# Kernel optimization log

Hardware: AMD Instinct MI355X
Metric: run time of the kernel (lower is better)

Reference implementation:

```python
import jax, jax.numpy as jnp
import numpy as np

BS, NQ, NK = 4096, 21, 7   # batch, num_neg queries, 7 keys (weekdays)
E = 512                     # key_size == query_size
H = 512                     # hidden_size
NEG_INF = -1e9


def setup_inputs() -> dict:
    key = jax.random.key(0)
    ks = jax.random.split(key, 6)
    sq = 1.0 / np.sqrt(E)
    sh = 1.0 / np.sqrt(H)
    return {
        "queries": jax.random.normal(ks[0], (BS, NQ, E), jnp.float32),
        "keys": jax.random.normal(ks[1], (BS, NK, E), jnp.float32),
        "wq_w": jax.random.normal(ks[2], (H, E), jnp.float32) * sq,
        "wq_b": jnp.zeros((H,), jnp.float32),
        "wk_w": jax.random.normal(ks[3], (H, E), jnp.float32) * sq,
        "wk_b": jnp.zeros((H,), jnp.float32),
        "wv_w": jax.random.normal(ks[4], (1, H), jnp.float32) * sh,
        "wv_b": jnp.zeros((1,), jnp.float32),
        "cum_subs_masks": jax.random.randint(ks[5], (BS, 1, NK, 1), 0, 2).astype(jnp.int32),
        "num_neg": NQ,
    }


def reference(queries, keys, wq_w, wq_b, wk_w, wk_b, wv_w, wv_b, cum_subs_masks, num_neg):
    # dropout p=0.0 -> identity (as in eval / p=0)
    q = jnp.einsum('bqe,he->bqh', queries, wq_w) + wq_b          # (bs,21,H)
    k = jnp.einsum('bke,he->bkh', keys, wk_w) + wk_b             # (bs,7,H)
    # additive score: broadcast q over keys, k over queries
    t = jnp.tanh(q[:, :, None, :] + k[:, None, :, :])            # (bs,21,7,H)
    scores = jnp.einsum('bqkh,oh->bqko', t, wv_w) + wv_b         # (bs,21,7,1)
    scores = scores + cum_subs_masks.astype(scores.dtype) * NEG_INF
    attn_weights = jax.nn.softmax(scores, axis=-2)               # softmax over 7 keys
    # weighted sum of the RAW keys (the module multiplies by expanded `keys`)
    attn_out = jnp.einsum('bqk,bke->bqe', attn_weights[..., 0], keys)  # (bs,21,E)
    return (attn_out, attn_weights)
```

## Files before the change

kernel.cpp:

```cpp
#include <hip/hip_runtime.h>
#include <hip/hip_bf16.h>

#define BS_   4096
#define NQ_   21
#define NK_   7
#define E_    512
#define MQ_   (BS_*NQ_)
#define MK_   (BS_*NK_)
#define MT1_  (MQ_/128)
#define MT2_  (MK_/128)
#define SCALE_ 2.88539008177792681f

typedef __attribute__((ext_vector_type(8))) short bf16x8;
typedef __attribute__((ext_vector_type(4))) float f32x4;
typedef __attribute__((ext_vector_type(8))) unsigned short u16x8;

__device__ __forceinline__ unsigned int cvt_pk_bf16(float lo, float hi){
  unsigned int r;
  asm("v_cvt_pk_bf16_f32 %0, %1, %2" : "=v"(r) : "v"(lo), "v"(hi));
  return r;
}
__device__ __forceinline__ unsigned short f2bfu(float x){
  return __builtin_bit_cast(unsigned short, __float2bfloat16(x));
}
__device__ __forceinline__ float bf2f(unsigned short h){
  return __builtin_bit_cast(float, (unsigned int)h << 16);
}
__device__ __forceinline__ void gload_lds16(const void* g, void* l){
  __builtin_amdgcn_global_load_lds(
      (const __attribute__((address_space(1))) unsigned int*)g,
      (__attribute__((address_space(3))) unsigned int*)l, 16, 0, 0);
}

__global__ __launch_bounds__(256) void cast_weights(
    const float* __restrict__ wq, const float* __restrict__ wk,
    unsigned int* __restrict__ oq, unsigned int* __restrict__ ok)
{
  int i = blockIdx.x * 256 + threadIdx.x;
  float4 a = ((const float4*)wq)[i];
  float4 b = ((const float4*)wk)[i];
  uint2 ua = { cvt_pk_bf16(a.x, a.y), cvt_pk_bf16(a.z, a.w) };
  uint2 ub = { cvt_pk_bf16(b.x, b.y), cvt_pk_bf16(b.z, b.w) };
  ((uint2*)oq)[i] = ua;
  ((uint2*)ok)[i] = ub;
}

__global__ __launch_bounds__(256)
void gemm_proj(const float* __restrict__ Aq, const float* __restrict__ Ak,
               const unsigned short* __restrict__ Bq, const unsigned short* __restrict__ Bk,
               const float* __restrict__ bq, const float* __restrict__ bk,
               unsigned short* __restrict__ Cq, unsigned short* __restrict__ Ck)
{
  __shared__ char Asm[2][128 * 128];
  __shared__ char Bsm[2][128 * 64];

  const int tid  = threadIdx.x;
  const int lane = tid & 63;
  const int w    = tid >> 6;
  const int wr   = w >> 1, wc = w & 1;

  const int orig = (int)blockIdx.x;
  const int j    = orig >> 3;
  int       mt   = (j >> 2) * 8 + (orig & 7);
  const int nt   = j & 3;

  const float* A; const unsigned short* Bw; const float* bias; unsigned short* C;
  if (mt < MT1_){ A = Aq; Bw = Bq; bias = bq; C = Cq; }
  else          { A = Ak; Bw = Bk; bias = bk; C = Ck; mt -= MT1_; }

  const long m0 = (long)mt << 7;
  const int  n0 = nt << 7;
  const char* Abyte = (const char*)(A + m0 * E_);
  const char* Bbyte = (const char*)Bw;

  long asrc[4]; int adst[4];
#pragma unroll
  for (int i = 0; i < 4; ++i){
    const int c   = tid + i * 256;
    const int row = c >> 3;
    const int sl  = c & 7;
    asrc[i] = (long)row * (E_ * 4) + ((sl * 16) ^ ((row & 7) << 4));
    adst[i] = c * 16;
  }
  long bsrc[2]; int bdst[2];
#pragma unroll
  for (int i = 0; i < 2; ++i){
    const int c   = tid + i * 256;
    const int row = c >> 2;
    const int sl  = c & 3;
    bsrc[i] = (long)(n0 + row) * (E_ * 2) + ((sl * 16) ^ (((row >> 1) & 3) << 4));
    bdst[i] = c * 16;
  }

  int aoff0[4], aoff1[4], boff[4];
#pragma unroll
  for (int m = 0; m < 4; ++m){
    const int r  = wr * 64 + m * 16 + (lane & 15);
    const int sw = (r & 7) << 4;
    aoff0[m] = r * 128 + ((32 * (lane >> 4)     ) ^ sw);
    aoff1[m] = r * 128 + ((32 * (lane >> 4) + 16) ^ sw);
  }
#pragma unroll
  for (int n = 0; n < 4; ++n){
    const int r = wc * 64 + n * 16 + (lane & 15);
    boff[n] = r * 64 + ((16 * (lane >> 4)) ^ (((r >> 1) & 3) << 4));
  }

  f32x4 acc[4][4];
  const f32x4 z4 = {0.f, 0.f, 0.f, 0.f};
#pragma unroll
  for (int m = 0; m < 4; ++m)
#pragma unroll
    for (int n = 0; n < 4; ++n) acc[m][n] = z4;

#pragma unroll
  for (int i = 0; i < 4; ++i) gload_lds16(Abyte + asrc[i], Asm[0] + adst[i]);
#pragma unroll
  for (int i = 0; i < 2; ++i) gload_lds16(Bbyte + bsrc[i], Bsm[0] + bdst[i]);
  __syncthreads();

  union U8 { unsigned short s[8]; bf16x8 v; };

#pragma unroll 2
  for (int t = 0; t < 16; ++t){
    const int buf = t & 1, nbuf = buf ^ 1;
    if (t < 15){
      const long ka = (long)(t + 1) * 128;
      const long kb = (long)(t + 1) * 64;
#pragma unroll
      for (int i = 0; i < 4; ++i) gload_lds16(Abyte + asrc[i] + ka, Asm[nbuf] + adst[i]);
#pragma unroll
      for (int i = 0; i < 2; ++i) gload_lds16(Bbyte + bsrc[i] + kb, Bsm[nbuf] + bdst[i]);
    }
    bf16x8 af[4], bfr[4];
#pragma unroll
    for (int m = 0; m < 4; ++m){
      f32x4 lo = *(const f32x4*)(Asm[buf] + aoff0[m]);
      f32x4 hi = *(const f32x4*)(Asm[buf] + aoff1[m]);
      U8 u;
      u.s[0] = f2bfu(lo[0]); u.s[1] = f2bfu(lo[1]);
      u.s[2] = f2bfu(lo[2]); u.s[3] = f2bfu(lo[3]);
      u.s[4] = f2bfu(hi[0]); u.s[5] = f2bfu(hi[1]);
      u.s[6] = f2bfu(hi[2]); u.s[7] = f2bfu(hi[3]);
      af[m] = u.v;
    }
#pragma unroll
    for (int n = 0; n < 4; ++n)
      bfr[n] = *(const bf16x8*)(Bsm[buf] + boff[n]);
#pragma unroll
    for (int m = 0; m < 4; ++m)
#pragma unroll
      for (int n = 0; n < 4; ++n)
        acc[m][n] = __builtin_amdgcn_mfma_f32_16x16x32_bf16(af[m], bfr[n], acc[m][n], 0, 0, 0);
    __syncthreads();
  }

  const int ccol0 = n0 + wc * 64 + (lane & 15);
  float bvs[4];
#pragma unroll
  for (int n = 0; n < 4; ++n) bvs[n] = bias[ccol0 + n * 16] * SCALE_;
#pragma unroll
  for (int m = 0; m < 4; ++m){
    const long rbase = m0 + wr * 64 + m * 16 + (lane >> 4) * 4;
#pragma unroll
    for (int n = 0; n < 4; ++n){
      const long col = ccol0 + n * 16;
      float v0 = fmaf(acc[m][n][0], SCALE_, bvs[n]);
      float v1 = fmaf(acc[m][n][1], SCALE_, bvs[n]);
      float v2 = fmaf(acc[m][n][2], SCALE_, bvs[n]);
      float v3 = fmaf(acc[m][n][3], SCALE_, bvs[n]);
      unsigned int u01 = cvt_pk_bf16(v0, v1);
      unsigned int u23 = cvt_pk_bf16(v2, v3);
      C[(rbase + 0) * E_ + col] = (unsigned short)(u01 & 0xffffu);
      C[(rbase + 1) * E_ + col] = (unsigned short)(u01 >> 16);
      C[(rbase + 2) * E_ + col] = (unsigned short)(u23 & 0xffffu);
      C[(rbase + 3) * E_ + col] = (unsigned short)(u23 >> 16);
    }
  }
}

__global__ __launch_bounds__(256, 2)
void attn_fused(const unsigned short* __restrict__ qp,
                const unsigned short* __restrict__ kp,
                const float* __restrict__ keys,
                const float* __restrict__ wv, const float* __restrict__ wvb,
                const int* __restrict__ mask,
                float* __restrict__ out0, float* __restrict__ out1)
{
  const int lane = threadIdx.x & 63;
  const int b    = blockIdx.x * 4 + (threadIdx.x >> 6);

  float wvr[8];
  *(float4*)&wvr[0] = ((const float4*)wv)[lane * 2];
  *(float4*)&wvr[4] = ((const float4*)wv)[lane * 2 + 1];

  float kf[NK_][8];
#pragma unroll
  for (int k = 0; k < NK_; ++k){
    u16x8 u = *(const u16x8*)(kp + ((long)b * NK_ + k) * E_ + lane * 8);
#pragma unroll
    for (int j = 0; j < 8; ++j) kf[k][j] = bf2f((unsigned short)u[j]);
  }
  float kr[NK_][8];
#pragma unroll
  for (int k = 0; k < NK_; ++k){
    const float4* p = (const float4*)(keys + ((long)b * NK_ + k) * E_ + lane * 8);
    *(float4*)&kr[k][0] = p[0];
    *(float4*)&kr[k][4] = p[1];
  }

  float wsum = ((wvr[0] + wvr[1]) + (wvr[2] + wvr[3])) + ((wvr[4] + wvr[5]) + (wvr[6] + wvr[7]));
#pragma unroll
  for (int off = 32; off; off >>= 1) wsum += __shfl_xor(wsum, off, 64);

  const float vb = wvb[0];
  float base[NK_];
#pragma unroll
  for (int k = 0; k < NK_; ++k)
    base[k] = (wsum + vb) + (float)mask[b * NK_ + k] * (-1e9f);

  const unsigned short* qrow = qp + (long)b * NQ_ * E_ + lane * 8;
  u16x8 qv = *(const u16x8*)qrow;

  float4* o0 = (float4*)(out0 + (long)b * NQ_ * E_) + lane * 2;
  float*  o1 = out1 + (long)b * (NQ_ * NK_);

  for (int qi = 0; qi < NQ_; ++qi){
    u16x8 qn = qv;
    if (qi < NQ_ - 1) qn = *(const u16x8*)(qrow + (qi + 1) * E_);

    float qf[8];
#pragma unroll
    for (int j = 0; j < 8; ++j) qf[j] = bf2f((unsigned short)qv[j]);
    qv = qn;

    float acc[NK_];
#pragma unroll
    for (int k = 0; k < NK_; ++k){
      float a = 0.f;
#pragma unroll
      for (int j = 0; j < 8; ++j){
        float x = qf[j] + kf[k][j];
        float e = __builtin_amdgcn_exp2f(x);
        float r = __builtin_amdgcn_rcpf(e + 1.0f);
        a = fmaf(wvr[j], r, a);
      }
      acc[k] = a;
    }
#pragma unroll
    for (int k = 0; k < NK_; ++k){
      float a = acc[k];
#pragma unroll
      for (int off = 32; off; off >>= 1) a += __shfl_xor(a, off, 64);
      acc[k] = a;
    }
    float sc[NK_], mx = -3.4e38f;
#pragma unroll
    for (int k = 0; k < NK_; ++k){ sc[k] = fmaf(-2.f, acc[k], base[k]); mx = fmaxf(mx, sc[k]); }
    float sum = 0.f;
#pragma unroll
    for (int k = 0; k < NK_; ++k){ sc[k] = __expf(sc[k] - mx); sum += sc[k]; }
    const float inv = __builtin_amdgcn_rcpf(sum);
    float wgt[NK_];
#pragma unroll
    for (int k = 0; k < NK_; ++k) wgt[k] = sc[k] * inv;

    float wsel = wgt[0];
#pragma unroll
    for (int k = 1; k < NK_; ++k) wsel = (lane == k) ? wgt[k] : wsel;
    if (lane < NK_) o1[qi * NK_ + lane] = wsel;

    float4 lo = {0.f,0.f,0.f,0.f}, hi = {0.f,0.f,0.f,0.f};
#pragma unroll
    for (int k = 0; k < NK_; ++k){
      lo.x = fmaf(wgt[k], kr[k][0], lo.x);
      lo.y = fmaf(wgt[k], kr[k][1], lo.y);
      lo.z = fmaf(wgt[k], kr[k][2], lo.z);
      lo.w = fmaf(wgt[k], kr[k][3], lo.w);
      hi.x = fmaf(wgt[k], kr[k][4], hi.x);
      hi.y = fmaf(wgt[k], kr[k][5], hi.y);
      hi.z = fmaf(wgt[k], kr[k][6], hi.z);
      hi.w = fmaf(wgt[k], kr[k][7], hi.w);
    }
    o0[qi * 128 + 0] = lo;
    o0[qi * 128 + 1] = hi;
  }
}

extern "C" void kernel_launch(void* const* d_in, const int* in_sizes, int n_in,
                              void* d_out, int out_size, void* d_ws, size_t ws_size,
                              hipStream_t stream)
{
  const float* queries = (const float*)d_in[0];
  const float* keys    = (const float*)d_in[1];
  const float* wq_w    = (const float*)d_in[2];
  const float* wq_b    = (const float*)d_in[3];
  const float* wk_w    = (const float*)d_in[4];
  const float* wk_b    = (const float*)d_in[5];
  const float* wv_w    = (const float*)d_in[6];
  const float* wv_b    = (const float*)d_in[7];
  const int*   mask    = (const int*)d_in[8];
  (void)in_sizes; (void)n_in; (void)out_size; (void)ws_size;

  float* out0 = (float*)d_out;
  float* out1 = out0 + (long)MQ_ * E_;

  char* ws = (char*)d_ws;
  unsigned short* wqb = (unsigned short*)ws;
  unsigned short* wkb = (unsigned short*)(ws + 512 * 512 * 2);
  unsigned short* qb  = (unsigned short*)(ws + (1 << 20));
  unsigned short* kb  = qb + (size_t)MQ_ * E_;

  cast_weights<<<dim3(256), dim3(256), 0, stream>>>(wq_w, wk_w, (unsigned int*)wqb, (unsigned int*)wkb);
  gemm_proj<<<dim3((MT1_ + MT2_) * 4), dim3(256), 0, stream>>>(
      queries, keys, wqb, wkb, wq_b, wk_b, qb, kb);
  attn_fused<<<dim3(BS_ / 4), dim3(256), 0, stream>>>(qb, kb, keys, wv_w, wv_b, mask, out0, out1);
}
```

Before: 250.0 us.

## Convert A tile to bf16 once on load instead of per-fragment LDS read

The A (activation) tile now goes global→register, is converted to bf16 with packed cvt, and is stored into LDS as bf16 with a new swizzle. The old path copied fp32 directly into LDS and converted element by element on every fragment read. This halves A's LDS footprint and read traffic and removes the scalar conversions from the MFMA inner loop. The cost is that A loads now pass through registers and the LDS store sits after the MFMAs. Launch bounds also request 4 blocks per CU to raise occupancy now that LDS use is smaller.

```diff
diff --git a/kernel.cpp b/kernel.cpp
--- a/kernel.cpp
+++ b/kernel.cpp
@@ -19,9 +19,6 @@
   unsigned int r;
   asm("v_cvt_pk_bf16_f32 %0, %1, %2" : "=v"(r) : "v"(lo), "v"(hi));
   return r;
-}
-__device__ __forceinline__ unsigned short f2bfu(float x){
-  return __builtin_bit_cast(unsigned short, __float2bfloat16(x));
 }
 __device__ __forceinline__ float bf2f(unsigned short h){
   return __builtin_bit_cast(float, (unsigned int)h << 16);
@@ -45,13 +42,13 @@
   ((uint2*)ok)[i] = ub;
 }
 
-__global__ __launch_bounds__(256)
+__global__ __launch_bounds__(256, 4)
 void gemm_proj(const float* __restrict__ Aq, const float* __restrict__ Ak,
                const unsigned short* __restrict__ Bq, const unsigned short* __restrict__ Bk,
                const float* __restrict__ bq, const float* __restrict__ bk,
                unsigned short* __restrict__ Cq, unsigned short* __restrict__ Ck)
 {
-  __shared__ char Asm[2][128 * 128];
+  __shared__ char Asm[2][128 * 64];
   __shared__ char Bsm[2][128 * 64];
 
   const int tid  = threadIdx.x;
@@ -79,8 +76,8 @@
     const int c   = tid + i * 256;
     const int row = c >> 3;
     const int sl  = c & 7;
-    asrc[i] = (long)row * (E_ * 4) + ((sl * 16) ^ ((row & 7) << 4));
-    adst[i] = c * 16;
+    asrc[i] = (long)row * (E_ * 4) + sl * 16;
+    adst[i] = row * 64 + (((sl & 6) * 8) ^ (((row >> 1) & 3) << 4)) + (sl & 1) * 8;
   }
   long bsrc[2]; int bdst[2];
 #pragma unroll
@@ -92,13 +89,11 @@
     bdst[i] = c * 16;
   }
 
-  int aoff0[4], aoff1[4], boff[4];
+  int aoff[4], boff[4];
 #pragma unroll
   for (int m = 0; m < 4; ++m){
-    const int r  = wr * 64 + m * 16 + (lane & 15);
-    const int sw = (r & 7) << 4;
-    aoff0[m] = r * 128 + ((32 * (lane >> 4)     ) ^ sw);
-    aoff1[m] = r * 128 + ((32 * (lane >> 4) + 16) ^ sw);
+    const int r = wr * 64 + m * 16 + (lane & 15);
+    aoff[m] = r * 64 + ((16 * (lane >> 4)) ^ (((r >> 1) & 3) << 4));
   }
 #pragma unroll
   for (int n = 0; n < 4; ++n){
@@ -113,45 +108,49 @@
 #pragma unroll
     for (int n = 0; n < 4; ++n) acc[m][n] = z4;
 
-#pragma unroll
-  for (int i = 0; i < 4; ++i) gload_lds16(Abyte + asrc[i], Asm[0] + adst[i]);
-#pragma unroll
-  for (int i = 0; i < 2; ++i) gload_lds16(Bbyte + bsrc[i], Bsm[0] + bdst[i]);
+  {
+    float4 av[4];
+#pragma unroll
+    for (int i = 0; i < 4; ++i) av[i] = *(const float4*)(Abyte + asrc[i]);
+#pragma unroll
+    for (int i = 0; i < 2; ++i) gload_lds16(Bbyte + bsrc[i], Bsm[0] + bdst[i]);
+#pragma unroll
+    for (int i = 0; i < 4; ++i){
+      uint2 u = { cvt_pk_bf16(av[i].x, av[i].y), cvt_pk_bf16(av[i].z, av[i].w) };
+      *(uint2*)(Asm[0] + adst[i]) = u;
+    }
+  }
   __syncthreads();
-
-  union U8 { unsigned short s[8]; bf16x8 v; };
 
 #pragma unroll 2
   for (int t = 0; t < 16; ++t){
     const int buf = t & 1, nbuf = buf ^ 1;
+    float4 av[4];
     if (t < 15){
       const long ka = (long)(t + 1) * 128;
       const long kb = (long)(t + 1) * 64;
 #pragma unroll
-      for (int i = 0; i < 4; ++i) gload_lds16(Abyte + asrc[i] + ka, Asm[nbuf] + adst[i]);
+      for (int i = 0; i < 4; ++i) av[i] = *(const float4*)(Abyte + asrc[i] + ka);
 #pragma unroll
       for (int i = 0; i < 2; ++i) gload_lds16(Bbyte + bsrc[i] + kb, Bsm[nbuf] + bdst[i]);
     }
     bf16x8 af[4], bfr[4];
 #pragma unroll
-    for (int m = 0; m < 4; ++m){
-      f32x4 lo = *(const f32x4*)(Asm[buf] + aoff0[m]);
-      f32x4 hi = *(const f32x4*)(Asm[buf] + aoff1[m]);
-      U8 u;
-      u.s[0] = f2bfu(lo[0]); u.s[1] = f2bfu(lo[1]);
-      u.s[2] = f2bfu(lo[2]); u.s[3] = f2bfu(lo[3]);
-      u.s[4] = f2bfu(hi[0]); u.s[5] = f2bfu(hi[1]);
-      u.s[6] = f2bfu(hi[2]); u.s[7] = f2bfu(hi[3]);
-      af[m] = u.v;
-    }
-#pragma unroll
-    for (int n = 0; n < 4; ++n)
-      bfr[n] = *(const bf16x8*)(Bsm[buf] + boff[n]);
+    for (int m = 0; m < 4; ++m) af[m]  = *(const bf16x8*)(Asm[buf] + aoff[m]);
+#pragma unroll
+    for (int n = 0; n < 4; ++n) bfr[n] = *(const bf16x8*)(Bsm[buf] + boff[n]);
 #pragma unroll
     for (int m = 0; m < 4; ++m)
 #pragma unroll
       for (int n = 0; n < 4; ++n)
         acc[m][n] = __builtin_amdgcn_mfma_f32_16x16x32_bf16(af[m], bfr[n], acc[m][n], 0, 0, 0);
+    if (t < 15){
+#pragma unroll
+      for (int i = 0; i < 4; ++i){
+        uint2 u = { cvt_pk_bf16(av[i].x, av[i].y), cvt_pk_bf16(av[i].z, av[i].w) };
+        *(uint2*)(Asm[nbuf] + adst[i]) = u;
+      }
+    }
     __syncthreads();
   }
 
```

New measurement: 251.6 us. About the same (+0.6%).
